# Optimization experiments

Hardware: AMD Instinct MI355X
Metric: run time of the kernel (lower is better)

Reference implementation:

```python
import jax, jax.numpy as jnp
import numpy as np

B_SZ, N_INST, D_IN, D_OUT, C_COMP, M_RANK = 512, 4, 1024, 1024, 64, 256

def setup_inputs() -> dict:
    key = jax.random.key(0)
    k1, k2, k3, k4 = jax.random.split(key, 4)
    x = jax.random.normal(k1, (B_SZ, N_INST, D_IN), dtype=jnp.float32)
    A = jax.random.normal(k2, (N_INST, C_COMP, D_IN, M_RANK), dtype=jnp.float32) * 0.02
    Bp = jax.random.normal(k3, (N_INST, C_COMP, M_RANK, D_OUT), dtype=jnp.float32) * 0.02
    topk_mask = jax.random.randint(k4, (B_SZ, N_INST, C_COMP), 0, 2, dtype=jnp.int32)
    return {"x": x, "A": A, "B": Bp, "topk_mask": topk_mask}

def reference(x, A, B, topk_mask):
    # inner: [b, i, C, m]
    inner = jnp.einsum('bid,icdm->bicm', x, A)
    inner = inner * topk_mask.astype(inner.dtype)[..., None]
    # comp: [b, i, C, d_out]
    comp = jnp.einsum('bicm,icmo->bico', inner, B)
    # sum over components C -> [b, i, d_out]
    return comp.sum(axis=2)
```

## Files before the change

kernel.cpp:

```cpp
#include <hip/hip_runtime.h>
#include <hip/hip_bf16.h>
#include <stdint.h>

#define B_SZ   512
#define NINST  4
#define D_IN   1024
#define D_OUTD 1024
#define CCOMP  64
#define MRANK  256
#define KTOT   (CCOMP*MRANK)

typedef __attribute__((ext_vector_type(4))) float  f32x4;
typedef __attribute__((ext_vector_type(8))) __bf16 bf16x8;
typedef __attribute__((ext_vector_type(4))) __bf16 bf16x4;

__device__ inline void gload_lds16(const __bf16* g, __bf16* l) {
  __builtin_amdgcn_global_load_lds(
      (const __attribute__((address_space(1))) void*)g,
      (__attribute__((address_space(3))) void*)l, 16, 0, 0);
}

__global__ __launch_bounds__(256)
void xcvt_kernel(const float* __restrict__ x, __bf16* __restrict__ xbf)
{
  const int total = (B_SZ*NINST*D_IN) / 4;
  for (int v = blockIdx.x*256 + threadIdx.x; v < total; v += gridDim.x*256) {
    const int k4 = v & 255;
    const int i  = (v >> 8) & 3;
    const int b  = v >> 10;
    f32x4 f = ((const f32x4*)x)[v];
    bf16x4 h; h[0]=(__bf16)f.x; h[1]=(__bf16)f.y; h[2]=(__bf16)f.z; h[3]=(__bf16)f.w;
    ((bf16x4*)xbf)[((size_t)i*B_SZ + b)*256 + k4] = h;
  }
}

__global__ __launch_bounds__(256, 2)
void p1_kernel(const __bf16* __restrict__ xbf, const float* __restrict__ A,
               const int* __restrict__ mask, __bf16* __restrict__ inner)
{
  const int bid = blockIdx.x;
  const int L   = (bid & 7) * 64 + (bid >> 3);
  const int bt  = L & 3;
  const int mt  = (L >> 2) & 1;
  const int icg = L >> 3;
  const int ic0 = icg * 4;
  const int i   = ic0 >> 6;
  const int c0  = ic0 & 63;
  const int b0  = bt * 128;
  const int m0  = mt * 128;

  const int tid  = threadIdx.x;
  const int lane = tid & 63;
  const int wid  = tid >> 6;
  const int wr   = wid >> 1;
  const int wc   = wid & 1;

  __shared__ __align__(16) char smem[65536];
  __bf16* Xs = (__bf16*)smem;
  __bf16* As = (__bf16*)(smem + 32768);

  f32x4 acc[4][4];
#pragma unroll
  for (int a_ = 0; a_ < 4; ++a_)
#pragma unroll
    for (int b_ = 0; b_ < 4; ++b_)
      acc[a_][b_] = (f32x4){0.f, 0.f, 0.f, 0.f};

  const __bf16* xbase  = xbf + ((size_t)i * B_SZ + b0) * D_IN;
  const float*  Abase0 = A + (size_t)ic0 * D_IN * MRANK + m0;

  const int bo = tid & 127;
  const int bg = tid >> 7;

  float areg[4][8];

  auto stageXs = [&](int buf, int kt) {
#pragma unroll
    for (int q = 0; q < 4; ++q) {
      const int ci  = wid*4 + q;
      const int row = ci*8 + (lane >> 3);
      const int kch = (lane & 7) ^ (row & 7);
      gload_lds16(xbase + (size_t)row * D_IN + (kt & 15)*64 + kch*8,
                  Xs + buf*8192 + ci*512);
    }
  };
  auto loadA = [&](int kt) {
    const float* Ab = Abase0 + (size_t)(kt >> 4) * D_IN * MRANK;
#pragma unroll
    for (int q = 0; q < 4; ++q)
#pragma unroll
      for (int j = 0; j < 8; ++j)
        areg[q][j] = Ab[(size_t)((kt & 15)*64 + (bg*4+q)*8 + j)*MRANK + bo];
  };
  auto writeA = [&](int buf) {
#pragma unroll
    for (int q = 0; q < 4; ++q) {
      const int oct = bg*4 + q;
      bf16x8 h;
#pragma unroll
      for (int j = 0; j < 8; ++j) h[j] = (__bf16)areg[q][j];
      *(bf16x8*)(As + buf*8192 + bo*64 + ((oct ^ (bo & 7)))*8) = h;
    }
  };

  stageXs(0, 0); loadA(0); writeA(0);
  __syncthreads();

  int cur = 0;
  for (int kt = 0; kt < 64; ++kt) {
    if (kt+1 < 64) { stageXs(cur ^ 1, kt+1); loadA(kt+1); }
#pragma unroll
    for (int kk = 0; kk < 2; ++kk) {
      const int oct = kk*4 + (lane >> 4);
      bf16x8 af[4];
#pragma unroll
      for (int mi = 0; mi < 4; ++mi) {
        const int row = wr*64 + mi*16 + (lane & 15);
        af[mi] = *(const bf16x8*)(Xs + cur*8192 + row*64 + ((oct ^ (row & 7)))*8);
      }
#pragma unroll
      for (int ni = 0; ni < 4; ++ni) {
        const int col = wc*64 + ni*16 + (lane & 15);
        bf16x8 bfr = *(const bf16x8*)(As + cur*8192 + col*64 + ((oct ^ (col & 7)))*8);
#pragma unroll
        for (int mi = 0; mi < 4; ++mi)
          acc[mi][ni] = __builtin_amdgcn_mfma_f32_16x16x32_bf16(af[mi], bfr, acc[mi][ni], 0, 0, 0);
      }
    }
    if ((kt & 15) == 15) {
      const int c = c0 + (kt >> 4);
      __bf16* obase = inner + ((size_t)i * B_SZ + b0) * KTOT + (size_t)c * MRANK + m0;
      float mv[16];
#pragma unroll
      for (int mi = 0; mi < 4; ++mi)
#pragma unroll
        for (int j = 0; j < 4; ++j) {
          const int row = wr*64 + mi*16 + (lane >> 4)*4 + j;
          mv[mi*4+j] = (float)mask[(size_t)(b0 + row) * (NINST*CCOMP) + i*CCOMP + c];
        }
#pragma unroll
      for (int mi = 0; mi < 4; ++mi)
#pragma unroll
        for (int ni = 0; ni < 4; ++ni) {
          const int colL = wc*64 + ni*16 + (lane & 15);
#pragma unroll
          for (int j = 0; j < 4; ++j) {
            const int rowL = wr*64 + mi*16 + (lane >> 4)*4 + j;
            obase[(size_t)rowL * KTOT + colL] = (__bf16)(acc[mi][ni][j] * mv[mi*4+j]);
          }
#pragma unroll
          for (int j = 0; j < 4; ++j) acc[mi][ni][j] = 0.f;
        }
    }
    if (kt+1 < 64) writeA(cur ^ 1);
    __syncthreads();
    cur ^= 1;
  }
}

__global__ __launch_bounds__(256, 2)
void p2_kernel(const __bf16* __restrict__ inner, const float* __restrict__ Bm,
               float* __restrict__ dst, int nks)
{
  const int bid = blockIdx.x;
  const int L   = (bid & 7) * (gridDim.x >> 3) + (bid >> 3);
  const int bt  = L & 3;
  const int nt  = (L >> 2) & 7;
  const int rest = L >> 5;
  const int ks  = rest % nks;
  const int i   = rest / nks;
  const int b0  = bt * 128;
  const int o0  = nt * 128;
  const int NSTEP = (KTOT/64) / nks;
  const int kb0   = ks * NSTEP;

  const int tid  = threadIdx.x;
  const int lane = tid & 63;
  const int wid  = tid >> 6;
  const int wr   = wid >> 1;
  const int wc   = wid & 1;

  __shared__ __align__(16) char smem[65536];
  __bf16* Is = (__bf16*)smem;
  __bf16* Bs = (__bf16*)(smem + 32768);

  f32x4 acc[4][4];
#pragma unroll
  for (int a_ = 0; a_ < 4; ++a_)
#pragma unroll
    for (int b_ = 0; b_ < 4; ++b_)
      acc[a_][b_] = (f32x4){0.f, 0.f, 0.f, 0.f};

  const __bf16* ibase = inner + ((size_t)i * B_SZ + b0) * KTOT;
  const float*  Bbase = Bm + (size_t)i * KTOT * D_OUTD + o0;

  const int bo = tid & 127;
  const int bg = tid >> 7;

  float breg[4][8];

  auto stageIs = [&](int buf, int kt) {
#pragma unroll
    for (int q = 0; q < 4; ++q) {
      const int ci  = wid*4 + q;
      const int row = ci*8 + (lane >> 3);
      const int kch = (lane & 7) ^ (row & 7);
      gload_lds16(ibase + (size_t)row * KTOT + kt*64 + kch*8,
                  Is + buf*8192 + ci*512);
    }
  };
  auto loadB = [&](int kt) {
#pragma unroll
    for (int q = 0; q < 4; ++q)
#pragma unroll
      for (int j = 0; j < 8; ++j)
        breg[q][j] = Bbase[(size_t)(kt*64 + (bg*4+q)*8 + j)*D_OUTD + bo];
  };
  auto writeB = [&](int buf) {
#pragma unroll
    for (int q = 0; q < 4; ++q) {
      const int oct = bg*4 + q;
      bf16x8 h;
#pragma unroll
      for (int j = 0; j < 8; ++j) h[j] = (__bf16)breg[q][j];
      *(bf16x8*)(Bs + buf*8192 + bo*64 + ((oct ^ (bo & 7)))*8) = h;
    }
  };

  stageIs(0, kb0); loadB(kb0); writeB(0);
  __syncthreads();

  int cur = 0;
  for (int t = 0; t < NSTEP; ++t) {
    if (t+1 < NSTEP) { stageIs(cur ^ 1, kb0 + t + 1); loadB(kb0 + t + 1); }
#pragma unroll
    for (int kk = 0; kk < 2; ++kk) {
      const int oct = kk*4 + (lane >> 4);
      bf16x8 af[4];
#pragma unroll
      for (int mi = 0; mi < 4; ++mi) {
        const int row = wr*64 + mi*16 + (lane & 15);
        af[mi] = *(const bf16x8*)(Is + cur*8192 + row*64 + ((oct ^ (row & 7)))*8);
      }
#pragma unroll
      for (int ni = 0; ni < 4; ++ni) {
        const int col = wc*64 + ni*16 + (lane & 15);
        bf16x8 bfr = *(const bf16x8*)(Bs + cur*8192 + col*64 + ((oct ^ (col & 7)))*8);
#pragma unroll
        for (int mi = 0; mi < 4; ++mi)
          acc[mi][ni] = __builtin_amdgcn_mfma_f32_16x16x32_bf16(af[mi], bfr, acc[mi][ni], 0, 0, 0);
      }
    }
    if (t+1 < NSTEP) writeB(cur ^ 1);
    __syncthreads();
    cur ^= 1;
  }

  float* obase = dst + (size_t)ks * ((size_t)B_SZ*NINST*D_OUTD)
               + ((size_t)b0 * NINST + i) * D_OUTD + o0;
#pragma unroll
  for (int mi = 0; mi < 4; ++mi)
#pragma unroll
    for (int ni = 0; ni < 4; ++ni) {
      const int colL = wc*64 + ni*16 + (lane & 15);
#pragma unroll
      for (int j = 0; j < 4; ++j) {
        const int rowL = wr*64 + mi*16 + (lane >> 4)*4 + j;
        obase[(size_t)rowL * (NINST*D_OUTD) + colL] = acc[mi][ni][j];
      }
    }
}

__global__ __launch_bounds__(256)
void reduce_kernel(const float* __restrict__ part, float* __restrict__ out, int nks)
{
  const int total = (B_SZ*NINST*D_OUTD) / 4;
  for (int v = blockIdx.x*256 + threadIdx.x; v < total; v += gridDim.x*256) {
    f32x4 s = ((const f32x4*)part)[v];
    for (int ks = 1; ks < nks; ++ks)
      s += ((const f32x4*)part)[(size_t)ks*total + v];
    ((f32x4*)out)[v] = s;
  }
}

extern "C" void kernel_launch(void* const* d_in, const int* in_sizes, int n_in,
                              void* d_out, int out_size, void* d_ws, size_t ws_size,
                              hipStream_t stream) {
  const float* x    = (const float*)d_in[0];
  const float* A    = (const float*)d_in[1];
  const float* Bm   = (const float*)d_in[2];
  const int*   mask = (const int*)d_in[3];

  const size_t innerB = (size_t)NINST * B_SZ * KTOT * 2;
  const size_t xbfB   = (size_t)NINST * B_SZ * D_IN * 2;
  const size_t partB  = (size_t)B_SZ * NINST * D_OUTD * 4;

  char* p = (char*)d_ws;
  __bf16* inner = (__bf16*)p;             p += innerB;
  __bf16* xbf   = (__bf16*)p;             p += xbfB;
  const size_t used = (size_t)(p - (char*)d_ws);

  int nks = 1;
  if      (ws_size >= used + 4*partB) nks = 4;
  else if (ws_size >= used + 2*partB) nks = 2;
  float* part = (nks > 1) ? (float*)p : (float*)d_out;

  xcvt_kernel<<<dim3(1024),  dim3(256), 0, stream>>>(x, xbf);
  p1_kernel<<<dim3(512),     dim3(256), 0, stream>>>(xbf, A, mask, inner);
  p2_kernel<<<dim3(128*nks), dim3(256), 0, stream>>>(inner, Bm, part, nks);
  if (nks > 1)
    reduce_kernel<<<dim3(512), dim3(256), 0, stream>>>(part, (float*)d_out, nks);
}
```

Baseline: 269.2 us.

## Stage fp32 A tiles asynchronously into LDS with triple buffering in p1

The p1 kernel now uses 512 threads per block and loads fp32 A tiles straight into LDS with global_load_lds into a three-slot ring, converting them to bf16 in LDS instead of loading them through registers. Explicit vmcnt/lgkmcnt waits and raw barriers let the A loads run two steps ahead of compute. The goal is to hide the strided global latency of A and cut register pressure. In exchange it needs about 144KB of LDS, limiting occupancy to one block per CU, and each step adds an LDS round trip for the conversion.

```diff
diff --git a/kernel.cpp b/kernel.cpp
--- a/kernel.cpp
+++ b/kernel.cpp
@@ -14,11 +14,27 @@
 typedef __attribute__((ext_vector_type(8))) __bf16 bf16x8;
 typedef __attribute__((ext_vector_type(4))) __bf16 bf16x4;
 
-__device__ inline void gload_lds16(const __bf16* g, __bf16* l) {
+__device__ inline void gload16(const void* g, void* l) {
   __builtin_amdgcn_global_load_lds(
       (const __attribute__((address_space(1))) void*)g,
       (__attribute__((address_space(3))) void*)l, 16, 0, 0);
 }
+
+#define BAR_LG() do { \
+  asm volatile("s_waitcnt lgkmcnt(0)" ::: "memory"); \
+  __builtin_amdgcn_sched_barrier(0); \
+  __builtin_amdgcn_s_barrier(); \
+  __builtin_amdgcn_sched_barrier(0); } while (0)
+#define BAR_V4() do { \
+  asm volatile("s_waitcnt lgkmcnt(0) vmcnt(4)" ::: "memory"); \
+  __builtin_amdgcn_sched_barrier(0); \
+  __builtin_amdgcn_s_barrier(); \
+  __builtin_amdgcn_sched_barrier(0); } while (0)
+#define BAR_V0() do { \
+  asm volatile("s_waitcnt lgkmcnt(0) vmcnt(0)" ::: "memory"); \
+  __builtin_amdgcn_sched_barrier(0); \
+  __builtin_amdgcn_s_barrier(); \
+  __builtin_amdgcn_sched_barrier(0); } while (0)
 
 __global__ __launch_bounds__(256)
 void xcvt_kernel(const float* __restrict__ x, __bf16* __restrict__ xbf)
@@ -34,7 +50,7 @@
   }
 }
 
-__global__ __launch_bounds__(256, 2)
+__global__ __launch_bounds__(512, 1)
 void p1_kernel(const __bf16* __restrict__ xbf, const float* __restrict__ A,
                const int* __restrict__ mask, __bf16* __restrict__ inner)
 {
@@ -52,16 +68,17 @@
   const int tid  = threadIdx.x;
   const int lane = tid & 63;
   const int wid  = tid >> 6;
-  const int wr   = wid >> 1;
-  const int wc   = wid & 1;
-
-  __shared__ __align__(16) char smem[65536];
-  __bf16* Xs = (__bf16*)smem;
-  __bf16* As = (__bf16*)(smem + 32768);
-
-  f32x4 acc[4][4];
-#pragma unroll
-  for (int a_ = 0; a_ < 4; ++a_)
+  const int wr   = wid & 3;
+  const int wc   = wid >> 2;
+
+  __shared__ __align__(16) char smem[147456];
+  __bf16* Xs  = (__bf16*)smem;
+  float*  fA  = (float*)(smem + 32768);
+  __bf16* bfA = (__bf16*)(smem + 131072);
+
+  f32x4 acc[2][4];
+#pragma unroll
+  for (int a_ = 0; a_ < 2; ++a_)
 #pragma unroll
     for (int b_ = 0; b_ < 4; ++b_)
       acc[a_][b_] = (f32x4){0.f, 0.f, 0.f, 0.f};
@@ -72,89 +89,96 @@
   const int bo = tid & 127;
   const int bg = tid >> 7;
 
-  float areg[4][8];
-
-  auto stageXs = [&](int buf, int kt) {
+  auto stageX = [&](int buf, int kt) {
+#pragma unroll
+    for (int q = 0; q < 2; ++q) {
+      const int u   = wid*2 + q;
+      const int row = u*8 + (lane >> 3);
+      const int kch = (lane & 7) ^ (row & 7);
+      gload16(xbase + (size_t)row * D_IN + (kt & 15)*64 + kch*8,
+              Xs + buf*8192 + u*512);
+    }
+  };
+  auto stageA32 = [&](int slot, int kt) {
+    const float* Ab = Abase0 + (size_t)(kt >> 4) * D_IN * MRANK;
 #pragma unroll
     for (int q = 0; q < 4; ++q) {
-      const int ci  = wid*4 + q;
-      const int row = ci*8 + (lane >> 3);
-      const int kch = (lane & 7) ^ (row & 7);
-      gload_lds16(xbase + (size_t)row * D_IN + (kt & 15)*64 + kch*8,
-                  Xs + buf*8192 + ci*512);
-    }
-  };
-  auto loadA = [&](int kt) {
-    const float* Ab = Abase0 + (size_t)(kt >> 4) * D_IN * MRANK;
-#pragma unroll
-    for (int q = 0; q < 4; ++q)
+      const int u = wid*4 + q;
+      const int d = u*2 + (lane >> 5);
+      gload16(Ab + (size_t)((kt & 15)*64 + d) * MRANK + (lane & 31)*4,
+              fA + slot*8192 + u*256);
+    }
+  };
+  auto cvtA = [&](int slot) {
+#pragma unroll
+    for (int q = 0; q < 2; ++q) {
+      const int oct = bg*2 + q;
+      bf16x8 h;
 #pragma unroll
       for (int j = 0; j < 8; ++j)
-        areg[q][j] = Ab[(size_t)((kt & 15)*64 + (bg*4+q)*8 + j)*MRANK + bo];
-  };
-  auto writeA = [&](int buf) {
-#pragma unroll
-    for (int q = 0; q < 4; ++q) {
-      const int oct = bg*4 + q;
-      bf16x8 h;
-#pragma unroll
-      for (int j = 0; j < 8; ++j) h[j] = (__bf16)areg[q][j];
-      *(bf16x8*)(As + buf*8192 + bo*64 + ((oct ^ (bo & 7)))*8) = h;
-    }
-  };
-
-  stageXs(0, 0); loadA(0); writeA(0);
-  __syncthreads();
-
-  int cur = 0;
-  for (int kt = 0; kt < 64; ++kt) {
-    if (kt+1 < 64) { stageXs(cur ^ 1, kt+1); loadA(kt+1); }
+        h[j] = (__bf16)fA[slot*8192 + (oct*8 + j)*128 + bo];
+      *(bf16x8*)(bfA + bo*64 + ((oct ^ (bo & 7)))*8) = h;
+    }
+  };
+  auto computeStep = [&](int xbuf) {
 #pragma unroll
     for (int kk = 0; kk < 2; ++kk) {
       const int oct = kk*4 + (lane >> 4);
-      bf16x8 af[4];
-#pragma unroll
-      for (int mi = 0; mi < 4; ++mi) {
-        const int row = wr*64 + mi*16 + (lane & 15);
-        af[mi] = *(const bf16x8*)(Xs + cur*8192 + row*64 + ((oct ^ (row & 7)))*8);
+      bf16x8 af[2];
+#pragma unroll
+      for (int mi = 0; mi < 2; ++mi) {
+        const int row = wr*32 + mi*16 + (lane & 15);
+        af[mi] = *(const bf16x8*)(Xs + xbuf*8192 + row*64 + ((oct ^ (row & 7)))*8);
       }
 #pragma unroll
       for (int ni = 0; ni < 4; ++ni) {
         const int col = wc*64 + ni*16 + (lane & 15);
-        bf16x8 bfr = *(const bf16x8*)(As + cur*8192 + col*64 + ((oct ^ (col & 7)))*8);
-#pragma unroll
-        for (int mi = 0; mi < 4; ++mi)
+        bf16x8 bfr = *(const bf16x8*)(bfA + col*64 + ((oct ^ (col & 7)))*8);
+#pragma unroll
+        for (int mi = 0; mi < 2; ++mi)
           acc[mi][ni] = __builtin_amdgcn_mfma_f32_16x16x32_bf16(af[mi], bfr, acc[mi][ni], 0, 0, 0);
       }
     }
-    if ((kt & 15) == 15) {
-      const int c = c0 + (kt >> 4);
-      __bf16* obase = inner + ((size_t)i * B_SZ + b0) * KTOT + (size_t)c * MRANK + m0;
-      float mv[16];
-#pragma unroll
-      for (int mi = 0; mi < 4; ++mi)
+  };
+  auto segEpilogue = [&](int kt) {
+    const int c = c0 + (kt >> 4);
+    __bf16* obase = inner + ((size_t)i * B_SZ + b0) * KTOT + (size_t)c * MRANK + m0;
+    float mv[8];
+#pragma unroll
+    for (int mi = 0; mi < 2; ++mi)
+#pragma unroll
+      for (int j = 0; j < 4; ++j) {
+        const int row = wr*32 + mi*16 + (lane >> 4)*4 + j;
+        mv[mi*4+j] = (float)mask[(size_t)(b0 + row) * (NINST*CCOMP) + i*CCOMP + c];
+      }
+#pragma unroll
+    for (int mi = 0; mi < 2; ++mi)
+#pragma unroll
+      for (int ni = 0; ni < 4; ++ni) {
+        const int colL = wc*64 + ni*16 + (lane & 15);
 #pragma unroll
         for (int j = 0; j < 4; ++j) {
-          const int row = wr*64 + mi*16 + (lane >> 4)*4 + j;
-          mv[mi*4+j] = (float)mask[(size_t)(b0 + row) * (NINST*CCOMP) + i*CCOMP + c];
+          const int rowL = wr*32 + mi*16 + (lane >> 4)*4 + j;
+          obase[(size_t)rowL * KTOT + colL] = (__bf16)(acc[mi][ni][j] * mv[mi*4+j]);
         }
 #pragma unroll
-      for (int mi = 0; mi < 4; ++mi)
-#pragma unroll
-        for (int ni = 0; ni < 4; ++ni) {
-          const int colL = wc*64 + ni*16 + (lane & 15);
-#pragma unroll
-          for (int j = 0; j < 4; ++j) {
-            const int rowL = wr*64 + mi*16 + (lane >> 4)*4 + j;
-            obase[(size_t)rowL * KTOT + colL] = (__bf16)(acc[mi][ni][j] * mv[mi*4+j]);
-          }
-#pragma unroll
-          for (int j = 0; j < 4; ++j) acc[mi][ni][j] = 0.f;
-        }
-    }
-    if (kt+1 < 64) writeA(cur ^ 1);
-    __syncthreads();
-    cur ^= 1;
+        for (int j = 0; j < 4; ++j) acc[mi][ni][j] = 0.f;
+      }
+  };
+
+  stageX(0, 0);
+  stageA32(0, 0);
+  stageA32(1, 1);
+  BAR_V4();
+
+  for (int t = 0; t < 64; ++t) {
+    if (t+1 < 64) stageX((t+1) & 1, t+1);
+    cvtA(t % 3);
+    BAR_LG();
+    computeStep(t & 1);
+    if ((t & 15) == 15) segEpilogue(t);
+    if (t+2 < 64) stageA32((t+2) % 3, t+2);
+    if (t < 63) { if (t < 62) BAR_V4(); else BAR_V0(); }
   }
 }
 
@@ -196,7 +220,6 @@
 
   const int bo = tid & 127;
   const int bg = tid >> 7;
-
   float breg[4][8];
 
   auto stageIs = [&](int buf, int kt) {
@@ -205,8 +228,8 @@
       const int ci  = wid*4 + q;
       const int row = ci*8 + (lane >> 3);
       const int kch = (lane & 7) ^ (row & 7);
-      gload_lds16(ibase + (size_t)row * KTOT + kt*64 + kch*8,
-                  Is + buf*8192 + ci*512);
+      gload16(ibase + (size_t)row * KTOT + kt*64 + kch*8,
+              Is + buf*8192 + ci*512);
     }
   };
   auto loadB = [&](int kt) {
@@ -306,7 +329,7 @@
   float* part = (nks > 1) ? (float*)p : (float*)d_out;
 
   xcvt_kernel<<<dim3(1024),  dim3(256), 0, stream>>>(x, xbf);
-  p1_kernel<<<dim3(512),     dim3(256), 0, stream>>>(xbf, A, mask, inner);
+  p1_kernel<<<dim3(512),     dim3(512), 0, stream>>>(xbf, A, mask, inner);
   p2_kernel<<<dim3(128*nks), dim3(256), 0, stream>>>(inner, Bm, part, nks);
   if (nks > 1)
     reduce_kernel<<<dim3(512), dim3(256), 0, stream>>>(part, (float*)d_out, nks);
```

Measured after the change: 283.9 us. +5.4%, slower.

## Enlarge p2 tiles to 256x256 with 512 threads and triple-buffered A staging

Applied to the files above, without the earlier changes.

Reworks the second GEMM kernel to use 256x256 output tiles with 8 waves per block, 160KB LDS, a three-slot async global-to-LDS pipeline for the inner activations, and partial vmcnt waits instead of full syncthreads. MFMA issue is wrapped in raised wave priority. Split-K is raised to 8 when workspace allows, and the reduce grid is doubled. The aim is more reuse per loaded byte and better overlap of loads with MFMA. The cost is one block per CU with heavy register and LDS use, and more partial-sum traffic from the deeper split.

```diff
diff --git a/kernel.cpp b/kernel.cpp
--- a/kernel.cpp
+++ b/kernel.cpp
@@ -14,11 +14,17 @@
 typedef __attribute__((ext_vector_type(8))) __bf16 bf16x8;
 typedef __attribute__((ext_vector_type(4))) __bf16 bf16x4;
 
-__device__ inline void gload_lds16(const __bf16* g, __bf16* l) {
+__device__ inline void gload16(const void* g, void* l) {
   __builtin_amdgcn_global_load_lds(
       (const __attribute__((address_space(1))) void*)g,
       (__attribute__((address_space(3))) void*)l, 16, 0, 0);
 }
+
+#define BARN(N) do { \
+  asm volatile("s_waitcnt lgkmcnt(0) vmcnt(" #N ")" ::: "memory"); \
+  __builtin_amdgcn_sched_barrier(0); \
+  __builtin_amdgcn_s_barrier(); \
+  __builtin_amdgcn_sched_barrier(0); } while (0)
 
 __global__ __launch_bounds__(256)
 void xcvt_kernel(const float* __restrict__ x, __bf16* __restrict__ xbf)
@@ -71,7 +77,6 @@
 
   const int bo = tid & 127;
   const int bg = tid >> 7;
-
   float areg[4][8];
 
   auto stageXs = [&](int buf, int kt) {
@@ -80,8 +85,8 @@
       const int ci  = wid*4 + q;
       const int row = ci*8 + (lane >> 3);
       const int kch = (lane & 7) ^ (row & 7);
-      gload_lds16(xbase + (size_t)row * D_IN + (kt & 15)*64 + kch*8,
-                  Xs + buf*8192 + ci*512);
+      gload16(xbase + (size_t)row * D_IN + (kt & 15)*64 + kch*8,
+              Xs + buf*8192 + ci*512);
     }
   };
   auto loadA = [&](int kt) {
@@ -158,35 +163,37 @@
   }
 }
 
-__global__ __launch_bounds__(256, 2)
+__global__ __launch_bounds__(512, 1)
 void p2_kernel(const __bf16* __restrict__ inner, const float* __restrict__ Bm,
                float* __restrict__ dst, int nks)
 {
   const int bid = blockIdx.x;
-  const int L   = (bid & 7) * (gridDim.x >> 3) + (bid >> 3);
-  const int bt  = L & 3;
-  const int nt  = (L >> 2) & 7;
-  const int rest = L >> 5;
+  const int nwg = gridDim.x;
+  const int L   = (bid & 7) * (nwg >> 3) + (bid >> 3);
+  const int tile = L & 7;
+  const int rest = L >> 3;
   const int ks  = rest % nks;
   const int i   = rest / nks;
-  const int b0  = bt * 128;
-  const int o0  = nt * 128;
+  const int mt  = tile & 1;
+  const int nt  = tile >> 1;
+  const int b0  = mt * 256;
+  const int o0  = nt * 256;
   const int NSTEP = (KTOT/64) / nks;
   const int kb0   = ks * NSTEP;
 
   const int tid  = threadIdx.x;
   const int lane = tid & 63;
   const int wid  = tid >> 6;
-  const int wr   = wid >> 1;
-  const int wc   = wid & 1;
-
-  __shared__ __align__(16) char smem[65536];
-  __bf16* Is = (__bf16*)smem;
-  __bf16* Bs = (__bf16*)(smem + 32768);
-
-  f32x4 acc[4][4];
-#pragma unroll
-  for (int a_ = 0; a_ < 4; ++a_)
+  const int wr   = wid >> 2;
+  const int wc   = wid & 3;
+
+  __shared__ __align__(16) char smem[163840];
+  __bf16* As = (__bf16*)smem;
+  __bf16* Bs = (__bf16*)(smem + 98304);
+
+  f32x4 acc[8][4];
+#pragma unroll
+  for (int a_ = 0; a_ < 8; ++a_)
 #pragma unroll
     for (int b_ = 0; b_ < 4; ++b_)
       acc[a_][b_] = (f32x4){0.f, 0.f, 0.f, 0.f};
@@ -194,19 +201,18 @@
   const __bf16* ibase = inner + ((size_t)i * B_SZ + b0) * KTOT;
   const float*  Bbase = Bm + (size_t)i * KTOT * D_OUTD + o0;
 
-  const int bo = tid & 127;
-  const int bg = tid >> 7;
-
+  const int bo = tid & 255;
+  const int bg = tid >> 8;
   float breg[4][8];
 
-  auto stageIs = [&](int buf, int kt) {
+  auto stageA = [&](int slot, int kt) {
 #pragma unroll
     for (int q = 0; q < 4; ++q) {
-      const int ci  = wid*4 + q;
-      const int row = ci*8 + (lane >> 3);
+      const int u   = wid*4 + q;
+      const int row = u*8 + (lane >> 3);
       const int kch = (lane & 7) ^ (row & 7);
-      gload_lds16(ibase + (size_t)row * KTOT + kt*64 + kch*8,
-                  Is + buf*8192 + ci*512);
+      gload16(ibase + (size_t)row * KTOT + (size_t)(kb0 + kt)*64 + kch*8,
+              As + slot*16384 + u*512);
     }
   };
   auto loadB = [&](int kt) {
@@ -214,7 +220,7 @@
     for (int q = 0; q < 4; ++q)
 #pragma unroll
       for (int j = 0; j < 8; ++j)
-        breg[q][j] = Bbase[(size_t)(kt*64 + (bg*4+q)*8 + j)*D_OUTD + bo];
+        breg[q][j] = Bbase[(size_t)((size_t)(kb0 + kt)*64 + (bg*4+q)*8 + j)*D_OUTD + bo];
   };
   auto writeB = [&](int buf) {
 #pragma unroll
@@ -223,49 +229,62 @@
       bf16x8 h;
 #pragma unroll
       for (int j = 0; j < 8; ++j) h[j] = (__bf16)breg[q][j];
-      *(bf16x8*)(Bs + buf*8192 + bo*64 + ((oct ^ (bo & 7)))*8) = h;
-    }
-  };
-
-  stageIs(0, kb0); loadB(kb0); writeB(0);
-  __syncthreads();
-
-  int cur = 0;
+      *(bf16x8*)(Bs + buf*16384 + bo*64 + ((oct ^ (bo & 7)))*8) = h;
+    }
+  };
+
+  stageA(0, 0);
+  stageA(1, 1);
+  loadB(0); writeB(0);
+  BARN(0);
+
   for (int t = 0; t < NSTEP; ++t) {
-    if (t+1 < NSTEP) { stageIs(cur ^ 1, kb0 + t + 1); loadB(kb0 + t + 1); }
+    const int aslot = t % 3;
+    const int bbuf  = t & 1;
+    if (t+2 < NSTEP) stageA((t+2) % 3, t+2);
+    if (t+1 < NSTEP) loadB(t+1);
 #pragma unroll
     for (int kk = 0; kk < 2; ++kk) {
       const int oct = kk*4 + (lane >> 4);
-      bf16x8 af[4];
-#pragma unroll
-      for (int mi = 0; mi < 4; ++mi) {
-        const int row = wr*64 + mi*16 + (lane & 15);
-        af[mi] = *(const bf16x8*)(Is + cur*8192 + row*64 + ((oct ^ (row & 7)))*8);
-      }
+      bf16x8 bf[4];
 #pragma unroll
       for (int ni = 0; ni < 4; ++ni) {
         const int col = wc*64 + ni*16 + (lane & 15);
-        bf16x8 bfr = *(const bf16x8*)(Bs + cur*8192 + col*64 + ((oct ^ (col & 7)))*8);
-#pragma unroll
-        for (int mi = 0; mi < 4; ++mi)
-          acc[mi][ni] = __builtin_amdgcn_mfma_f32_16x16x32_bf16(af[mi], bfr, acc[mi][ni], 0, 0, 0);
-      }
-    }
-    if (t+1 < NSTEP) writeB(cur ^ 1);
-    __syncthreads();
-    cur ^= 1;
+        bf[ni] = *(const bf16x8*)(Bs + bbuf*16384 + col*64 + ((oct ^ (col & 7)))*8);
+      }
+#pragma unroll
+      for (int mh = 0; mh < 2; ++mh) {
+        bf16x8 af[4];
+#pragma unroll
+        for (int mi = 0; mi < 4; ++mi) {
+          const int row = wr*128 + (mh*4 + mi)*16 + (lane & 15);
+          af[mi] = *(const bf16x8*)(As + aslot*16384 + row*64 + ((oct ^ (row & 7)))*8);
+        }
+        __builtin_amdgcn_s_setprio(1);
+#pragma unroll
+        for (int ni = 0; ni < 4; ++ni)
+#pragma unroll
+          for (int mi = 0; mi < 4; ++mi)
+            acc[mh*4+mi][ni] = __builtin_amdgcn_mfma_f32_16x16x32_bf16(
+                af[mi], bf[ni], acc[mh*4+mi][ni], 0, 0, 0);
+        __builtin_amdgcn_s_setprio(0);
+      }
+    }
+    if (t+1 < NSTEP) writeB(bbuf ^ 1);
+    if (t+2 < NSTEP) BARN(4);
+    else             BARN(0);
   }
 
   float* obase = dst + (size_t)ks * ((size_t)B_SZ*NINST*D_OUTD)
                + ((size_t)b0 * NINST + i) * D_OUTD + o0;
 #pragma unroll
-  for (int mi = 0; mi < 4; ++mi)
+  for (int mi = 0; mi < 8; ++mi)
 #pragma unroll
     for (int ni = 0; ni < 4; ++ni) {
       const int colL = wc*64 + ni*16 + (lane & 15);
 #pragma unroll
       for (int j = 0; j < 4; ++j) {
-        const int rowL = wr*64 + mi*16 + (lane >> 4)*4 + j;
+        const int rowL = wr*128 + mi*16 + (lane >> 4)*4 + j;
         obase[(size_t)rowL * (NINST*D_OUTD) + colL] = acc[mi][ni][j];
       }
     }
@@ -301,13 +320,14 @@
   const size_t used = (size_t)(p - (char*)d_ws);
 
   int nks = 1;
-  if      (ws_size >= used + 4*partB) nks = 4;
+  if      (ws_size >= used + 8*partB) nks = 8;
+  else if (ws_size >= used + 4*partB) nks = 4;
   else if (ws_size >= used + 2*partB) nks = 2;
   float* part = (nks > 1) ? (float*)p : (float*)d_out;
 
   xcvt_kernel<<<dim3(1024),  dim3(256), 0, stream>>>(x, xbf);
   p1_kernel<<<dim3(512),     dim3(256), 0, stream>>>(xbf, A, mask, inner);
-  p2_kernel<<<dim3(128*nks), dim3(256), 0, stream>>>(inner, Bm, part, nks);
+  p2_kernel<<<dim3(32*nks),  dim3(512), 0, stream>>>(inner, Bm, part, nks);
   if (nks > 1)
-    reduce_kernel<<<dim3(512), dim3(256), 0, stream>>>(part, (float*)d_out, nks);
-}
+    reduce_kernel<<<dim3(1024), dim3(256), 0, stream>>>(part, (float*)d_out, nks);
+}
```

After: 259.2 us. -3.7%, faster.
